# Kernel optimization log

Measured on AMD Instinct MI355X. Metric: run time of the kernel, lower is better.

Reference implementation:

```python
import jax, jax.numpy as jnp
import numpy as np

B, N, DIN, DMID, DOUT, E = 64, 5000, 64, 128, 32, 80000


def setup_inputs() -> dict:
    key = jax.random.key(0)
    ks = jax.random.split(key, 12)
    p = lambda k, shape: jax.random.normal(k, shape, jnp.float32) * 0.05
    return {
        "x": jax.random.normal(ks[0], (B, N, DIN), jnp.float32),
        "edge_index": jax.random.randint(ks[1], (2, E), 0, N),
        "prev_hidden_state": jax.random.normal(ks[2], (B, N, DMID), jnp.float32),
        # GCNConv weights/biases for gates z, r, h
        "Wg_z": p(ks[3], (DIN, DMID)), "bg_z": jnp.zeros((DMID,), jnp.float32),
        "Wg_r": p(ks[4], (DIN, DMID)), "bg_r": jnp.zeros((DMID,), jnp.float32),
        "Wg_h": p(ks[5], (DIN, DMID)), "bg_h": jnp.zeros((DMID,), jnp.float32),
        # gate Linear layers on concat([conv_out, H]) -> DMID
        "Wl_z": p(ks[6], (2 * DMID, DMID)), "bl_z": jnp.zeros((DMID,), jnp.float32),
        "Wl_r": p(ks[7], (2 * DMID, DMID)), "bl_r": jnp.zeros((DMID,), jnp.float32),
        "Wl_h": p(ks[8], (2 * DMID, DMID)), "bl_h": jnp.zeros((DMID,), jnp.float32),
        # final output Linear
        "W_out": p(ks[9], (DMID, DOUT)), "b_out": jnp.zeros((DOUT,), jnp.float32),
    }


def reference(x, edge_index, prev_hidden_state,
              Wg_z, bg_z, Wg_r, bg_r, Wg_h, bg_h,
              Wl_z, bl_z, Wl_r, bl_r, Wl_h, bl_h,
              W_out, b_out):
    # GCN symmetric normalization with self-loops (pyg gcn_norm, improved=False)
    row, col = edge_index[0], edge_index[1]
    loop = jnp.arange(N)
    src = jnp.concatenate([row, loop])          # [E+N]
    dst = jnp.concatenate([col, loop])          # [E+N]
    ew = jnp.ones((E + N,), x.dtype)
    deg = jnp.zeros((N,), x.dtype).at[dst].add(ew)
    dis = jnp.where(deg > 0, jax.lax.rsqrt(jnp.maximum(deg, 1e-12)), 0.0)
    norm = dis[src] * ew * dis[dst]             # [E+N]

    def gcn(w, b):
        xw = jnp.einsum('bnd,de->bne', x, w)            # [B,N,DMID]
        msg = xw[:, src, :] * norm[None, :, None]       # gather + weight
        out = jnp.zeros((B, N, w.shape[1]), x.dtype).at[:, dst, :].add(msg)
        return out + b

    H = prev_hidden_state
    Z = jax.nn.sigmoid(jnp.concatenate([gcn(Wg_z, bg_z), H], -1) @ Wl_z + bl_z)
    R = jax.nn.sigmoid(jnp.concatenate([gcn(Wg_r, bg_r), H], -1) @ Wl_r + bl_r)
    Ht = jnp.tanh(jnp.concatenate([gcn(Wg_h, bg_h), H * R], -1) @ Wl_h + bl_h)
    H_new = Z * H + (1.0 - Z) * Ht                      # [B,N,DMID]

    y = jnp.mean(H_new, axis=1)                         # MeanAggregation over nodes
    y = jax.nn.relu(y) @ W_out + b_out                  # [B,DOUT]
    return (y, H_new)
```

## Files before the change

### kernel.cpp

```cpp
#include <hip/hip_runtime.h>
#include <cmath>

namespace {

constexpr int B = 64, N = 5000, DIN = 64, DMID = 128, DOUT = 32, E = 80000;
constexpr int NT = (N + 63) / 64;

typedef unsigned short u16;
typedef __attribute__((ext_vector_type(8))) short short8;
typedef __attribute__((ext_vector_type(4))) float floatx4;

#define MFMA16(a, b, c) __builtin_amdgcn_mfma_f32_16x16x32_bf16((a), (b), (c), 0, 0, 0)

__device__ __forceinline__ u16 f2bf(float f) {
  union { float f; unsigned u; } v; v.f = f;
  unsigned r = v.u + 0x7FFFu + ((v.u >> 16) & 1u);
  return (u16)(r >> 16);
}
__device__ __forceinline__ float bf2f(u16 s) {
  union { unsigned u; float f; } v; v.u = ((unsigned)s) << 16;
  return v.f;
}
__device__ __forceinline__ float sigmoid_fast(float x) {
  return __builtin_amdgcn_rcpf(1.f + __expf(-x));
}
__device__ __forceinline__ float tanh_fast(float x) {
  return fmaf(2.f, __builtin_amdgcn_rcpf(1.f + __expf(-2.f * x)), -1.f);
}


__global__ void count_kernel(const int* __restrict__ ei, int* counts) {
  int e = blockIdx.x * 256 + threadIdx.x;
  if (e < E) atomicAdd(&counts[ei[E + e]], 1);
}

__global__ void scan_kernel(int* counts, int* rowptr, float* dis) {
  __shared__ int sdata[1024];
  const int tid = threadIdx.x;
  constexpr int CH = (N + 1023) / 1024;
  int local[CH], cnt[CH];
  int s = 0;
  for (int i = 0; i < CH; i++) {
    int idx = tid * CH + i;
    int c = (idx < N) ? counts[idx] : 0;
    cnt[i] = c;
    local[i] = s;
    s += c;
  }
  sdata[tid] = s;
  __syncthreads();
  for (int off = 1; off < 1024; off <<= 1) {
    int v = (tid >= off) ? sdata[tid - off] : 0;
    __syncthreads();
    sdata[tid] += v;
    __syncthreads();
  }
  int prev = (tid > 0) ? sdata[tid - 1] : 0;
  for (int i = 0; i < CH; i++) {
    int idx = tid * CH + i;
    if (idx < N) {
      rowptr[idx] = prev + local[i];
      dis[idx] = rsqrtf((float)(cnt[i] + 1));
      counts[idx] = 0;
    }
  }
  if (tid == 1023) rowptr[N] = sdata[1023];
}

__global__ void fill_kernel(const int* __restrict__ ei, const int* __restrict__ rowptr,
                            const float* __restrict__ dis, int* counts,
                            int* csr_src, float* csr_w) {
  int e = blockIdx.x * 256 + threadIdx.x;
  if (e >= E) return;
  int r = ei[e], c = ei[E + e];
  int pos = rowptr[c] + atomicAdd(&counts[c], 1);
  csr_src[pos] = r;
  csr_w[pos] = dis[r] * dis[c];
}


__global__ void pack_kernel(const float* Wgz, const float* Wgr, const float* Wgh,
                            const float* Wlz, const float* Wlr, const float* Wlh,
                            const float* bgz, const float* bgr, const float* bgh,
                            const float* blz, const float* blr, const float* blh,
                            u16* wcB, u16* whB, float* bcAll) {
  int t = blockIdx.x * 256 + threadIdx.x;
  const float* Wg[3] = {Wgz, Wgr, Wgh};
  const float* Wl[3] = {Wlz, Wlr, Wlh};
  const float* bg[3] = {bgz, bgr, bgh};
  const float* bl[3] = {blz, blr, blh};
  if (t < 48 * 64) {
    int chunk = t >> 6, lane = t & 63;
    int q = lane >> 4, lm = lane & 15;
    int g = chunk >> 4, rem = chunk & 15, kt = rem >> 3, nt = rem & 7;
    int n = nt * 16 + lm;
#pragma unroll
    for (int jj = 0; jj < 8; jj++) {
      int k = kt * 32 + q * 8 + jj;
      float acc = 0.f;
      for (int j = 0; j < DMID; j++)
        acc = fmaf(Wg[g][k * DMID + j], Wl[g][j * DMID + n], acc);
      wcB[(size_t)(chunk * 64 + lane) * 8 + jj] = f2bf(acc);
    }
  } else if (t < 48 * 64 + 96 * 64) {
    int t2 = t - 48 * 64;
    int chunk = t2 >> 6, lane = t2 & 63;
    int q = lane >> 4, lm = lane & 15;
    int g = chunk >> 5, rem = chunk & 31, kt = rem >> 3, nt = rem & 7;
    int n = nt * 16 + lm;
#pragma unroll
    for (int jj = 0; jj < 8; jj++) {
      int k = kt * 32 + q * 8 + jj;
      whB[(size_t)t2 * 8 + jj] = f2bf(Wl[g][(DMID + k) * DMID + n]);
    }
  } else {
    int t3 = t - 48 * 64 - 96 * 64;
    if (t3 < 384) {
      int g = t3 >> 7, n = t3 & 127;
      float acc = bl[g][n];
      for (int j = 0; j < DMID; j++)
        acc = fmaf(bg[g][j], Wl[g][j * DMID + n], acc);
      bcAll[t3] = acc;
    }
  }
}


__global__ __launch_bounds__(256) void agg_kernel(
    const float* __restrict__ x, const int* __restrict__ rowptr,
    const int* __restrict__ csr_src, const float* __restrict__ csr_w,
    const float* __restrict__ dis, u16* __restrict__ xs) {
  constexpr int G = B * N / 16;
  const int bid = blockIdx.x;
  const int nb = (bid & 7) * (G >> 3) + (bid >> 3);
  const int sub = threadIdx.x >> 4;
  const int l16 = threadIdx.x & 15;
  const int unit = nb * 16 + sub;
  const int b = unit / N;
  const int n = unit - b * N;
  const float* xb = x + (size_t)b * N * DIN;
  const float d = dis[n];
  float4 v = *(const float4*)(xb + (size_t)n * DIN + l16 * 4);
  const float sw = d * d;
  float ax = v.x * sw, ay = v.y * sw, az = v.z * sw, aw = v.w * sw;
  const int s1 = rowptr[n + 1];
  int p = rowptr[n];
  for (; p + 4 <= s1; p += 4) {
    int i0 = csr_src[p], i1 = csr_src[p + 1], i2 = csr_src[p + 2], i3 = csr_src[p + 3];
    float w0 = csr_w[p], w1 = csr_w[p + 1], w2 = csr_w[p + 2], w3 = csr_w[p + 3];
    float4 a0 = *(const float4*)(xb + (size_t)i0 * DIN + l16 * 4);
    float4 a1 = *(const float4*)(xb + (size_t)i1 * DIN + l16 * 4);
    float4 a2 = *(const float4*)(xb + (size_t)i2 * DIN + l16 * 4);
    float4 a3 = *(const float4*)(xb + (size_t)i3 * DIN + l16 * 4);
    ax = fmaf(a0.x, w0, ax); ay = fmaf(a0.y, w0, ay);
    az = fmaf(a0.z, w0, az); aw = fmaf(a0.w, w0, aw);
    ax = fmaf(a1.x, w1, ax); ay = fmaf(a1.y, w1, ay);
    az = fmaf(a1.z, w1, az); aw = fmaf(a1.w, w1, aw);
    ax = fmaf(a2.x, w2, ax); ay = fmaf(a2.y, w2, ay);
    az = fmaf(a2.z, w2, az); aw = fmaf(a2.w, w2, aw);
    ax = fmaf(a3.x, w3, ax); ay = fmaf(a3.y, w3, ay);
    az = fmaf(a3.z, w3, az); aw = fmaf(a3.w, w3, aw);
  }
  for (; p < s1; p++) {
    int i0 = csr_src[p];
    float w0 = csr_w[p];
    float4 a0 = *(const float4*)(xb + (size_t)i0 * DIN + l16 * 4);
    ax = fmaf(a0.x, w0, ax); ay = fmaf(a0.y, w0, ay);
    az = fmaf(a0.z, w0, az); aw = fmaf(a0.w, w0, aw);
  }
  uint2 o;
  o.x = (unsigned)f2bf(ax) | ((unsigned)f2bf(ay) << 16);
  o.y = (unsigned)f2bf(az) | ((unsigned)f2bf(aw) << 16);
  *(uint2*)(xs + (size_t)unit * DIN + l16 * 4) = o;
}


constexpr int SH = 136;

__global__ __launch_bounds__(256, 4) void fused_mfma(
    const u16* __restrict__ xs, const float* __restrict__ H,
    const u16* __restrict__ wcB, const u16* __restrict__ whB,
    const float* __restrict__ bcAll,
    float* __restrict__ hnew, float* __restrict__ partials) {
  __shared__ u16 H_s[64 * SH];

  const int tid = threadIdx.x;
  const int b = blockIdx.y;
  const int n0 = blockIdx.x * 64;
  const int lane = tid & 63, w = tid >> 6;
  const int q = lane >> 4, lm = lane & 15;
  const int w16 = w * 16;

#pragma unroll
  for (int j = 0; j < 8; j++) {
    int idx = j * 64 + lane;
    int rl = idx >> 5, seg = idx & 31;
    int row = w16 + rl;
    float4 v = make_float4(0.f, 0.f, 0.f, 0.f);
    if (n0 + row < N) v = *(const float4*)(H + ((size_t)b * N + n0 + row) * DMID + seg * 4);
    uint2 p;
    p.x = (unsigned)f2bf(v.x) | ((unsigned)f2bf(v.y) << 16);
    p.y = (unsigned)f2bf(v.z) | ((unsigned)f2bf(v.w) << 16);
    *(uint2*)&H_s[row * SH + seg * 4] = p;
  }

  const int an = n0 + w16 + lm;
  short8 ax[2];
  if (an < N) {
    const u16* xrow = xs + ((size_t)b * N + an) * DIN;
    ax[0] = *(const short8*)(xrow + q * 8);
    ax[1] = *(const short8*)(xrow + 32 + q * 8);
  } else {
    ax[0] = short8{0, 0, 0, 0, 0, 0, 0, 0};
    ax[1] = short8{0, 0, 0, 0, 0, 0, 0, 0};
  }

  short8 ah[4];
#pragma unroll
  for (int kt = 0; kt < 4; kt++)
    ah[kt] = *(const short8*)&H_s[(w16 + lm) * SH + kt * 32 + q * 8];

  uint2 hstash[8];
#pragma unroll
  for (int nt = 0; nt < 8; nt++) {
    floatx4 a = {0.f, 0.f, 0.f, 0.f};
#pragma unroll
    for (int kt = 0; kt < 2; kt++)
      a = MFMA16(ax[kt], *(const short8*)(wcB + (size_t)((16 + kt * 8 + nt) * 64 + lane) * 8), a);
#pragma unroll
    for (int kt = 0; kt < 4; kt++)
      a = MFMA16(ah[kt], *(const short8*)(whB + (size_t)((32 + kt * 8 + nt) * 64 + lane) * 8), a);
    float bias = bcAll[128 + nt * 16 + lm];
    unsigned hx = 0u, hy = 0u;
#pragma unroll
    for (int r = 0; r < 4; r++) {
      int row = w16 + q * 4 + r, col = nt * 16 + lm;
      u16 hb = H_s[row * SH + col];
      float h = bf2f(hb);
      float rg = sigmoid_fast(a[r] + bias);
      H_s[row * SH + col] = f2bf(h * rg);
      if (r < 2) hx |= ((unsigned)hb) << (16 * r);
      else       hy |= ((unsigned)hb) << (16 * (r - 2));
    }
    hstash[nt] = make_uint2(hx, hy);
  }

  short8 ahr[4];
#pragma unroll
  for (int kt = 0; kt < 4; kt++)
    ahr[kt] = *(const short8*)&H_s[(w16 + lm) * SH + kt * 32 + q * 8];

#pragma unroll
  for (int nt = 0; nt < 8; nt++) {
    floatx4 za = {0.f, 0.f, 0.f, 0.f}, ha = {0.f, 0.f, 0.f, 0.f};
#pragma unroll
    for (int kt = 0; kt < 2; kt++) {
      za = MFMA16(ax[kt], *(const short8*)(wcB + (size_t)((0 + kt * 8 + nt) * 64 + lane) * 8), za);
      ha = MFMA16(ax[kt], *(const short8*)(wcB + (size_t)((32 + kt * 8 + nt) * 64 + lane) * 8), ha);
    }
#pragma unroll
    for (int kt = 0; kt < 4; kt++) {
      za = MFMA16(ah[kt], *(const short8*)(whB + (size_t)((0 + kt * 8 + nt) * 64 + lane) * 8), za);
      ha = MFMA16(ahr[kt], *(const short8*)(whB + (size_t)((64 + kt * 8 + nt) * 64 + lane) * 8), ha);
    }
    float zb = bcAll[nt * 16 + lm], hb_ = bcAll[256 + nt * 16 + lm];
    float colsum = 0.f;
#pragma unroll
    for (int r = 0; r < 4; r++) {
      int row = w16 + q * 4 + r;
      bool valid = (n0 + row) < N;
      unsigned word = (r < 2) ? hstash[nt].x : hstash[nt].y;
      float h = bf2f((u16)(word >> (16 * (r & 1))));
      float z = sigmoid_fast(za[r] + zb);
      float ht = tanh_fast(ha[r] + hb_);
      float hn = fmaf(z, h - ht, ht);
      if (valid) {
        hnew[((size_t)b * N + n0 + row) * DMID + nt * 16 + lm] = hn;
        colsum += hn;
      }
    }
    colsum += __shfl_xor(colsum, 16);
    colsum += __shfl_xor(colsum, 32);
    if (lane < 16)
      partials[(((size_t)b * NT + blockIdx.x) * 4 + w) * DMID + nt * 16 + lane] = colsum;
  }
}


__global__ void out_kernel(const float* __restrict__ partials, const float* __restrict__ Wout,
                           const float* __restrict__ bout, float* __restrict__ y) {
  const int b = blockIdx.x;
  const int c = threadIdx.x;
  __shared__ float m[DMID];
  float acc = 0.f;
  for (int t = 0; t < NT * 4; t++)
    acc += partials[((size_t)b * NT * 4 + t) * DMID + c];
  m[c] = fmaxf(acc * (1.f / (float)N), 0.f);
  __syncthreads();
  if (c < DOUT) {
    float a2 = bout[c];
    for (int jj = 0; jj < DMID; jj++)
      a2 = fmaf(m[jj], Wout[jj * DOUT + c], a2);
    y[b * DOUT + c] = a2;
  }
}

}

extern "C" void kernel_launch(void* const* d_in, const int* in_sizes, int n_in,
                              void* d_out, int out_size, void* d_ws, size_t ws_size,
                              hipStream_t stream) {
  const float* x = (const float*)d_in[0];
  const int* ei = (const int*)d_in[1];
  const float* H = (const float*)d_in[2];
  const float* Wgz = (const float*)d_in[3];
  const float* bgz = (const float*)d_in[4];
  const float* Wgr = (const float*)d_in[5];
  const float* bgr = (const float*)d_in[6];
  const float* Wgh = (const float*)d_in[7];
  const float* bgh = (const float*)d_in[8];
  const float* Wlz = (const float*)d_in[9];
  const float* blz = (const float*)d_in[10];
  const float* Wlr = (const float*)d_in[11];
  const float* blr = (const float*)d_in[12];
  const float* Wlh = (const float*)d_in[13];
  const float* blh = (const float*)d_in[14];
  const float* Wout = (const float*)d_in[15];
  const float* bout = (const float*)d_in[16];

  float* y = (float*)d_out;
  float* hnew = (float*)d_out + (size_t)B * DOUT;

  char* p = (char*)d_ws;
  auto carve = [&](size_t bytes) {
    char* q = p;
    p += (bytes + 255) & ~size_t(255);
    return q;
  };
  int* counts = (int*)carve((size_t)N * 4);
  int* rowptr = (int*)carve((size_t)(N + 1) * 4);
  int* csr_src = (int*)carve((size_t)E * 4);
  float* csr_w = (float*)carve((size_t)E * 4);
  float* dis = (float*)carve((size_t)N * 4);
  u16* wcB = (u16*)carve((size_t)48 * 64 * 8 * 2);
  u16* whB = (u16*)carve((size_t)96 * 64 * 8 * 2);
  float* bcAll = (float*)carve((size_t)384 * 4);
  float* partials = (float*)carve((size_t)B * NT * 4 * DMID * 4);
  u16* xs = (u16*)carve((size_t)B * N * DIN * 2);

  hipMemsetAsync(counts, 0, (size_t)N * 4, stream);
  pack_kernel<<<38, 256, 0, stream>>>(Wgz, Wgr, Wgh, Wlz, Wlr, Wlh,
                                      bgz, bgr, bgh, blz, blr, blh,
                                      wcB, whB, bcAll);
  count_kernel<<<(E + 255) / 256, 256, 0, stream>>>(ei, counts);
  scan_kernel<<<1, 1024, 0, stream>>>(counts, rowptr, dis);
  fill_kernel<<<(E + 255) / 256, 256, 0, stream>>>(ei, rowptr, dis, counts, csr_src, csr_w);
  agg_kernel<<<B * N / 16, 256, 0, stream>>>(x, rowptr, csr_src, csr_w, dis, xs);
  fused_mfma<<<dim3(NT, B), 256, 0, stream>>>(xs, H, wcB, whB, bcAll, hnew, partials);
  out_kernel<<<B, DMID, 0, stream>>>(partials, Wout, bout, y);
}
```

Before: 702.6 us.

## Fuse sparse aggregation into the MFMA gate kernel via shared memory

Removes the separate aggregation kernel and its bf16 intermediate buffer. Each fused block now gathers neighbor features for its 64-node tile, writes the aggregated rows to a new shared-memory tile, and reads MFMA A operands from there. The grid becomes 1D with an interleaved block-to-(batch, tile) mapping meant for cache locality. This saves a global write and read of B*N*DIN bf16 values and one launch. In exchange the irregular gather latency now sits inside the MFMA kernel, which may hurt its latency hiding and occupancy.

```diff
diff --git a/kernel.cpp b/kernel.cpp
--- a/kernel.cpp
+++ b/kernel.cpp
@@ -5,6 +5,7 @@
 
 constexpr int B = 64, N = 5000, DIN = 64, DMID = 128, DOUT = 32, E = 80000;
 constexpr int NT = (N + 63) / 64;
+constexpr int TOT = NT * B;
 
 typedef unsigned short u16;
 typedef __attribute__((ext_vector_type(8))) short short8;
@@ -126,70 +127,75 @@
 }
 
 
-__global__ __launch_bounds__(256) void agg_kernel(
+constexpr int SH = 136;
+constexpr int SX = 72;
+
+__global__ __launch_bounds__(256, 4) void fused_mfma(
     const float* __restrict__ x, const int* __restrict__ rowptr,
     const int* __restrict__ csr_src, const float* __restrict__ csr_w,
-    const float* __restrict__ dis, u16* __restrict__ xs) {
-  constexpr int G = B * N / 16;
-  const int bid = blockIdx.x;
-  const int nb = (bid & 7) * (G >> 3) + (bid >> 3);
-  const int sub = threadIdx.x >> 4;
-  const int l16 = threadIdx.x & 15;
-  const int unit = nb * 16 + sub;
-  const int b = unit / N;
-  const int n = unit - b * N;
-  const float* xb = x + (size_t)b * N * DIN;
-  const float d = dis[n];
-  float4 v = *(const float4*)(xb + (size_t)n * DIN + l16 * 4);
-  const float sw = d * d;
-  float ax = v.x * sw, ay = v.y * sw, az = v.z * sw, aw = v.w * sw;
-  const int s1 = rowptr[n + 1];
-  int p = rowptr[n];
-  for (; p + 4 <= s1; p += 4) {
-    int i0 = csr_src[p], i1 = csr_src[p + 1], i2 = csr_src[p + 2], i3 = csr_src[p + 3];
-    float w0 = csr_w[p], w1 = csr_w[p + 1], w2 = csr_w[p + 2], w3 = csr_w[p + 3];
-    float4 a0 = *(const float4*)(xb + (size_t)i0 * DIN + l16 * 4);
-    float4 a1 = *(const float4*)(xb + (size_t)i1 * DIN + l16 * 4);
-    float4 a2 = *(const float4*)(xb + (size_t)i2 * DIN + l16 * 4);
-    float4 a3 = *(const float4*)(xb + (size_t)i3 * DIN + l16 * 4);
-    ax = fmaf(a0.x, w0, ax); ay = fmaf(a0.y, w0, ay);
-    az = fmaf(a0.z, w0, az); aw = fmaf(a0.w, w0, aw);
-    ax = fmaf(a1.x, w1, ax); ay = fmaf(a1.y, w1, ay);
-    az = fmaf(a1.z, w1, az); aw = fmaf(a1.w, w1, aw);
-    ax = fmaf(a2.x, w2, ax); ay = fmaf(a2.y, w2, ay);
-    az = fmaf(a2.z, w2, az); aw = fmaf(a2.w, w2, aw);
-    ax = fmaf(a3.x, w3, ax); ay = fmaf(a3.y, w3, ay);
-    az = fmaf(a3.z, w3, az); aw = fmaf(a3.w, w3, aw);
-  }
-  for (; p < s1; p++) {
-    int i0 = csr_src[p];
-    float w0 = csr_w[p];
-    float4 a0 = *(const float4*)(xb + (size_t)i0 * DIN + l16 * 4);
-    ax = fmaf(a0.x, w0, ax); ay = fmaf(a0.y, w0, ay);
-    az = fmaf(a0.z, w0, az); aw = fmaf(a0.w, w0, aw);
-  }
-  uint2 o;
-  o.x = (unsigned)f2bf(ax) | ((unsigned)f2bf(ay) << 16);
-  o.y = (unsigned)f2bf(az) | ((unsigned)f2bf(aw) << 16);
-  *(uint2*)(xs + (size_t)unit * DIN + l16 * 4) = o;
-}
-
-
-constexpr int SH = 136;
-
-__global__ __launch_bounds__(256, 4) void fused_mfma(
-    const u16* __restrict__ xs, const float* __restrict__ H,
+    const float* __restrict__ dis, const float* __restrict__ H,
     const u16* __restrict__ wcB, const u16* __restrict__ whB,
     const float* __restrict__ bcAll,
     float* __restrict__ hnew, float* __restrict__ partials) {
   __shared__ u16 H_s[64 * SH];
+  __shared__ u16 XS_s[64 * SX];
 
   const int tid = threadIdx.x;
-  const int b = blockIdx.y;
-  const int n0 = blockIdx.x * 64;
+  const int bid = blockIdx.x;
+  const int nb = (bid & 7) * (TOT >> 3) + (bid >> 3);
+  const int b = nb / NT;
+  const int tile = nb - b * NT;
+  const int n0 = tile * 64;
   const int lane = tid & 63, w = tid >> 6;
   const int q = lane >> 4, lm = lane & 15;
   const int w16 = w * 16;
+
+  {
+    const int l16 = lane & 15;
+    const int rsub = lane >> 4;
+    const float* xbb = x + (size_t)b * N * DIN;
+#pragma unroll
+    for (int pass = 0; pass < 4; pass++) {
+      int rl = pass * 4 + rsub;
+      int n = n0 + w16 + rl;
+      float ax_ = 0.f, ay_ = 0.f, az_ = 0.f, aw_ = 0.f;
+      if (n < N) {
+        float d = dis[n];
+        float sw = d * d;
+        float4 v = *(const float4*)(xbb + (size_t)n * DIN + l16 * 4);
+        ax_ = v.x * sw; ay_ = v.y * sw; az_ = v.z * sw; aw_ = v.w * sw;
+        const int s1 = rowptr[n + 1];
+        int p = rowptr[n];
+        for (; p + 4 <= s1; p += 4) {
+          int i0 = csr_src[p], i1 = csr_src[p + 1], i2 = csr_src[p + 2], i3 = csr_src[p + 3];
+          float w0 = csr_w[p], w1 = csr_w[p + 1], w2 = csr_w[p + 2], w3 = csr_w[p + 3];
+          float4 a0 = *(const float4*)(xbb + (size_t)i0 * DIN + l16 * 4);
+          float4 a1 = *(const float4*)(xbb + (size_t)i1 * DIN + l16 * 4);
+          float4 a2 = *(const float4*)(xbb + (size_t)i2 * DIN + l16 * 4);
+          float4 a3 = *(const float4*)(xbb + (size_t)i3 * DIN + l16 * 4);
+          ax_ = fmaf(a0.x, w0, ax_); ay_ = fmaf(a0.y, w0, ay_);
+          az_ = fmaf(a0.z, w0, az_); aw_ = fmaf(a0.w, w0, aw_);
+          ax_ = fmaf(a1.x, w1, ax_); ay_ = fmaf(a1.y, w1, ay_);
+          az_ = fmaf(a1.z, w1, az_); aw_ = fmaf(a1.w, w1, aw_);
+          ax_ = fmaf(a2.x, w2, ax_); ay_ = fmaf(a2.y, w2, ay_);
+          az_ = fmaf(a2.z, w2, az_); aw_ = fmaf(a2.w, w2, aw_);
+          ax_ = fmaf(a3.x, w3, ax_); ay_ = fmaf(a3.y, w3, ay_);
+          az_ = fmaf(a3.z, w3, az_); aw_ = fmaf(a3.w, w3, aw_);
+        }
+        for (; p < s1; p++) {
+          int i0 = csr_src[p];
+          float w0 = csr_w[p];
+          float4 a0 = *(const float4*)(xbb + (size_t)i0 * DIN + l16 * 4);
+          ax_ = fmaf(a0.x, w0, ax_); ay_ = fmaf(a0.y, w0, ay_);
+          az_ = fmaf(a0.z, w0, az_); aw_ = fmaf(a0.w, w0, aw_);
+        }
+      }
+      uint2 o;
+      o.x = (unsigned)f2bf(ax_) | ((unsigned)f2bf(ay_) << 16);
+      o.y = (unsigned)f2bf(az_) | ((unsigned)f2bf(aw_) << 16);
+      *(uint2*)&XS_s[(w16 + rl) * SX + l16 * 4] = o;
+    }
+  }
 
 #pragma unroll
   for (int j = 0; j < 8; j++) {
@@ -204,17 +210,10 @@
     *(uint2*)&H_s[row * SH + seg * 4] = p;
   }
 
-  const int an = n0 + w16 + lm;
   short8 ax[2];
-  if (an < N) {
-    const u16* xrow = xs + ((size_t)b * N + an) * DIN;
-    ax[0] = *(const short8*)(xrow + q * 8);
-    ax[1] = *(const short8*)(xrow + 32 + q * 8);
-  } else {
-    ax[0] = short8{0, 0, 0, 0, 0, 0, 0, 0};
-    ax[1] = short8{0, 0, 0, 0, 0, 0, 0, 0};
-  }
-
+#pragma unroll
+  for (int kt = 0; kt < 2; kt++)
+    ax[kt] = *(const short8*)&XS_s[(w16 + lm) * SX + kt * 32 + q * 8];
   short8 ah[4];
 #pragma unroll
   for (int kt = 0; kt < 4; kt++)
@@ -282,7 +281,7 @@
     colsum += __shfl_xor(colsum, 16);
     colsum += __shfl_xor(colsum, 32);
     if (lane < 16)
-      partials[(((size_t)b * NT + blockIdx.x) * 4 + w) * DMID + nt * 16 + lane] = colsum;
+      partials[(((size_t)b * NT + tile) * 4 + w) * DMID + nt * 16 + lane] = colsum;
   }
 }
 
@@ -346,7 +345,6 @@
   u16* whB = (u16*)carve((size_t)96 * 64 * 8 * 2);
   float* bcAll = (float*)carve((size_t)384 * 4);
   float* partials = (float*)carve((size_t)B * NT * 4 * DMID * 4);
-  u16* xs = (u16*)carve((size_t)B * N * DIN * 2);
 
   hipMemsetAsync(counts, 0, (size_t)N * 4, stream);
   pack_kernel<<<38, 256, 0, stream>>>(Wgz, Wgr, Wgh, Wlz, Wlr, Wlh,
@@ -355,7 +353,7 @@
   count_kernel<<<(E + 255) / 256, 256, 0, stream>>>(ei, counts);
   scan_kernel<<<1, 1024, 0, stream>>>(counts, rowptr, dis);
   fill_kernel<<<(E + 255) / 256, 256, 0, stream>>>(ei, rowptr, dis, counts, csr_src, csr_w);
-  agg_kernel<<<B * N / 16, 256, 0, stream>>>(x, rowptr, csr_src, csr_w, dis, xs);
-  fused_mfma<<<dim3(NT, B), 256, 0, stream>>>(xs, H, wcB, whB, bcAll, hnew, partials);
+  fused_mfma<<<TOT, 256, 0, stream>>>(x, rowptr, csr_src, csr_w, dis, H,
+                                      wcB, whB, bcAll, hnew, partials);
   out_kernel<<<B, DMID, 0, stream>>>(partials, Wout, bout, y);
 }
```

Result: slower. 751.3 us (+6.9%).
